# Performance work log

Hardware: AMD Instinct MI355X
Metric: run time of the kernel (lower is better)

Reference implementation:

```python
import jax, jax.numpy as jnp
import numpy as np


def setup_inputs() -> dict:
    key = jax.random.key(0)
    k = jax.random.split(key, 5)
    C, Cb = 128, 64
    x = jax.random.normal(k[0], (8, C, 64, 64), dtype=jnp.float32)
    s_in = 1.0 / np.sqrt(C)
    s_b = 1.0 / np.sqrt(Cb)
    w_theta = jax.random.normal(k[1], (Cb, C), dtype=jnp.float32) * s_in
    w_phi = jax.random.normal(k[2], (Cb, C), dtype=jnp.float32) * s_in
    w_g = jax.random.normal(k[3], (Cb, C), dtype=jnp.float32) * s_in
    w_last = jax.random.normal(k[4], (C, Cb), dtype=jnp.float32) * s_b
    return {"x": x, "w_theta": w_theta, "w_phi": w_phi, "w_g": w_g, "w_last": w_last}


def reference(x, w_theta, w_phi, w_g, w_last):
    B, C, H, W = x.shape
    xf = x.reshape(B, C, H * W)            # [B, C, N]
    theta = jnp.einsum('kc,bcn->bkn', w_theta, xf)   # [B, Cb, N]
    phi = jnp.einsum('kc,bcn->bkn', w_phi, xf)       # [B, Cb, N]
    g = jnp.einsum('kc,bcn->bkn', w_g, xf)           # [B, Cb, N]
    # attention over spatial positions: [B, N, N]
    attn = jax.nn.softmax(jnp.einsum('bkn,bkm->bnm', theta, phi), axis=-1)
    y = jnp.einsum('bnm,bkm->bkn', attn, g)          # [B, Cb, N]
    out = jnp.einsum('ck,bkn->bcn', w_last, y).reshape(B, C, H, W)
    return out + x
```

## Files before the change

### kernel.cpp

```cpp
#include <hip/hip_runtime.h>
#include <stdint.h>

typedef _Float16 h8v __attribute__((ext_vector_type(8)));
typedef _Float16 h4v __attribute__((ext_vector_type(4)));
typedef float f4v __attribute__((ext_vector_type(4)));
typedef _Float16 f16;

#define NB 8
#define CC 128
#define CB 64
#define NN 4096
#define L2E 1.4426950408889634f

#define GLD(gp, lp) __builtin_amdgcn_global_load_lds( \
    (const __attribute__((address_space(1))) void*)(gp), \
    (__attribute__((address_space(3))) void*)(lp), 16, 0, 0)

#define WAITV1() asm volatile("s_waitcnt vmcnt(1)" ::: "memory")
#define WAITV0() asm volatile("s_waitcnt vmcnt(0)" ::: "memory")
#define WAITL0() asm volatile("s_waitcnt lgkmcnt(0)" ::: "memory")

__global__ __launch_bounds__(256) void pack_w(
    const float* __restrict__ wth, const float* __restrict__ wph,
    const float* __restrict__ wg,  const float* __restrict__ wl,
    f16* __restrict__ wthp, f16* __restrict__ wphp,
    f16* __restrict__ wgp,  f16* __restrict__ wlp)
{
    const int t = blockIdx.x * 256 + threadIdx.x;
    for (int i = t; i < 8192; i += 2048){
        const int j = i & 7, lane = (i >> 3) & 63, kc = (i >> 9) & 3, ks = i >> 11;
        const int row = ks * 16 + (lane & 15);
        const int col = kc * 32 + ((lane >> 4) & 3) * 8 + j;
        wthp[i] = (f16)(wth[row * CC + col] * L2E);
        wphp[i] = (f16)(wph[row * CC + col]);
        wgp [i] = (f16)(wg [row * CC + col]);
    }
    for (int i = t; i < 8192; i += 2048){
        const int j = i & 7, lane = (i >> 3) & 63, kc = (i >> 9) & 1, cs = i >> 10;
        const int row = cs * 16 + (lane & 15);
        const int col = kc * 32 + ((lane >> 4) & 3) * 8 + j;
        wlp[i] = (f16)(wl[row * CB + col]);
    }
}

__global__ __launch_bounds__(512) void proj_kernel(
    const float* __restrict__ x, const f16* __restrict__ wthp,
    const f16* __restrict__ wphp, const f16* __restrict__ wgp,
    f16* __restrict__ thetaT, f16* __restrict__ phiT, f16* __restrict__ gbuf)
{
    __shared__ __align__(16) f16 xT[64][136];
    __shared__ __align__(16) f16 rep[8][16 * 72];
    const int b  = blockIdx.x & 7;
    const int n0 = (blockIdx.x >> 3) << 6;
    const int t  = threadIdx.x;

    #pragma unroll
    for (int i = 0; i < 4; i++){
        int v  = t + 512 * i;
        int c  = v >> 4;
        int j0 = (v & 15) << 2;
        const f4v xv = *(const f4v*)&x[((size_t)(b * CC + c)) * NN + n0 + j0];
        #pragma unroll
        for (int jj = 0; jj < 4; jj++) xT[j0 + jj][c] = (f16)xv[jj];
    }
    __syncthreads();

    const int w = t >> 6, lane = t & 63, quad = lane >> 4, l15 = lane & 15;
    const int wq = w & 3, grp = w >> 2;
    const int rrow = lane >> 3, rcol = (lane & 7) * 8;

    h8v bx[4];
    #pragma unroll
    for (int kc = 0; kc < 4; kc++)
        bx[kc] = *(const h8v*)&xT[wq * 16 + l15][kc * 32 + quad * 8];

    {
        const f16* WP = (grp == 0) ? wthp : wphp;
        f16* OUT      = (grp == 0) ? thetaT : phiT;
        for (int ks = 0; ks < 4; ks++){
            f4v acc = {0.f, 0.f, 0.f, 0.f};
            #pragma unroll
            for (int kc = 0; kc < 4; kc++){
                const h8v af = *(const h8v*)&WP[(ks * 4 + kc) * 512 + lane * 8];
                acc = __builtin_amdgcn_mfma_f32_16x16x32_f16(af, bx[kc], acc, 0, 0, 0);
            }
            h4v pv;
            #pragma unroll
            for (int r = 0; r < 4; r++) pv[r] = (f16)acc[r];
            *(h4v*)&rep[w][l15 * 72 + ks * 16 + quad * 4] = pv;
        }
        #pragma unroll
        for (int j = 0; j < 2; j++){
            const h8v vv = *(const h8v*)&rep[w][(rrow + 8 * j) * 72 + rcol];
            *(h8v*)&OUT[((size_t)(b * NN + n0 + wq * 16 + rrow + 8 * j)) * CB + rcol] = vv;
        }
    }
    __syncthreads();

    h8v bw[4];
    #pragma unroll
    for (int kc = 0; kc < 4; kc++)
        bw[kc] = *(const h8v*)&wgp[(wq * 4 + kc) * 512 + lane * 8];
    #pragma unroll
    for (int ns2 = 0; ns2 < 2; ns2++){
        const int ns = grp * 2 + ns2;
        f4v acc = {0.f, 0.f, 0.f, 0.f};
        #pragma unroll
        for (int kc = 0; kc < 4; kc++){
            const h8v af = *(const h8v*)&xT[ns * 16 + l15][kc * 32 + quad * 8];
            acc = __builtin_amdgcn_mfma_f32_16x16x32_f16(af, bw[kc], acc, 0, 0, 0);
        }
        h4v pv;
        #pragma unroll
        for (int r = 0; r < 4; r++) pv[r] = (f16)acc[r];
        *(h4v*)&rep[wq][l15 * 72 + ns * 16 + quad * 4] = pv;
    }
    __syncthreads();
    {
        const int row = rrow + 8 * grp;
        const h8v vv = *(const h8v*)&rep[wq][row * 72 + rcol];
        *(h8v*)&gbuf[((size_t)(b * CB + wq * 16 + row)) * NN + n0 + rcol] = vv;
    }
}

__global__ __launch_bounds__(512, 4) void attn_kernel(
    const f16* __restrict__ thetaT, const f16* __restrict__ phiT,
    const f16* __restrict__ gbuf, const f16* __restrict__ wlp,
    const float* __restrict__ x, float* __restrict__ out)
{
    __shared__ __align__(16) char SM[49152];
    f16*   const PH  = (f16*)SM;
    f16*   const GG  = (f16*)(SM + 24576);
    float* const MG  = (float*)SM;
    float* const ML  = (float*)(SM + 17408);
    float* const FO  = (float*)SM;
    f16*   const YY  = (f16*)(SM + 36864);

    const int b  = blockIdx.x & 7;
    const int q0 = (blockIdx.x >> 3) << 6;
    const int t  = threadIdx.x;
    const int w  = t >> 6;
    const int lane = t & 63, quad = lane >> 4, l15 = lane & 15;
    const int wq = w & 3;
    const int h  = w >> 2;
    const int n0 = q0 + wq * 16;

    const size_t trow = ((size_t)(b * NN + n0 + l15)) * CB;
    const h8v a0 = *(const h8v*)&thetaT[trow + quad * 8];
    const h8v a1 = *(const h8v*)&thetaT[trow + 32 + quad * 8];

    const int srow = t >> 3;
    const int skg  = t & 7;
    const f16* pS = phiT + ((size_t)(b * NN + srow)) * CB + (skg ^ (srow & 7)) * 8;
    const f16* pG = gbuf + ((size_t)(b * CB + srow)) * NN + skg * 8;
    const int sgs = (srow >> 1) & 3;
    const int cA  = (2 * (skg & 3)) & 3;
    const int gdA = (skg >> 2) * 2048 + srow * 32 + ((cA      ^ sgs) * 8) + ((skg >> 1) & 1) * 4;
    const int gdB = (skg >> 2) * 2048 + srow * 32 + (((cA | 1) ^ sgs) * 8) + ((skg >> 1) & 1) * 4;

    const int so0 = (quad ^ (l15 & 7)) * 8;
    const int so1 = so0 ^ 32;
    const int gvs = (quad ^ ((l15 >> 1) & 3)) * 8;

    const f16* const PB0 = PH + h * 2048 + l15 * 64 + so0;
    const f16* const PB1 = PH + h * 2048 + l15 * 64 + so1;
    const f16* const GB  = GG + h * 2048 + l15 * 32 + gvs;
    f16* const WA = GG + gdA;
    f16* const WB = GG + gdB;
    f16* const PD = PH + t * 8;

    h8v gA = *(const h8v*)pG;
    h8v gB = *(const h8v*)(pG + 64);
    GLD(pS,                    PD);
    GLD(pS + (size_t)64 * CB,  PD + 4096);
    pG += 128;
    pS += (size_t)128 * CB;
    {
        h4v lo_, hi_;
        #pragma unroll
        for (int j = 0; j < 4; j++){ lo_[j] = gA[j]; hi_[j] = gA[4 + j]; }
        *(h4v*)&WA[0] = lo_;
        *(h4v*)&WB[0] = hi_;
    }

    float mrun = -1e30f, lrun = 0.f;
    const f4v zf = {0.f, 0.f, 0.f, 0.f};
    f4v o[4];
    #pragma unroll
    for (int tt = 0; tt < 4; tt++) o[tt] = zf;

#define STEPK(RC, V1, DO_W, DO_L, gw, gl) do {                              \
    if (V1) WAITV1(); else WAITV0();                                        \
    WAITL0();                                                               \
    __builtin_amdgcn_s_barrier();                                           \
    asm volatile("" ::: "memory");                                          \
    if (DO_W){                                                              \
        h4v lo_, hi_;                                                       \
        _Pragma("unroll")                                                   \
        for (int j = 0; j < 4; j++){ lo_[j] = gw[j]; hi_[j] = gw[4 + j]; }  \
        *(h4v*)&WA[((RC + 1) % 3) * 4096] = lo_;                            \
        *(h4v*)&WB[((RC + 1) % 3) * 4096] = hi_;                            \
    }                                                                       \
    if (DO_L){                                                              \
        gl = *(const h8v*)pG;  pG += 64;                                    \
        __builtin_amdgcn_sched_barrier(0);                                  \
        GLD(pS, PD + ((RC + 2) % 3) * 4096);                                \
        pS += (size_t)64 * CB;                                              \
    }                                                                       \
    f4v s0_, s1_;                                                           \
    __builtin_amdgcn_s_setprio(1);                                          \
    {                                                                       \
        const h8v pb0 = *(const h8v*)(PB0 + RC * 4096);                     \
        const h8v pb1 = *(const h8v*)(PB1 + RC * 4096);                     \
        f4v sv = zf;                                                        \
        sv = __builtin_amdgcn_mfma_f32_16x16x32_f16(pb0, a0, sv, 0, 0, 0);  \
        sv = __builtin_amdgcn_mfma_f32_16x16x32_f16(pb1, a1, sv, 0, 0, 0);  \
        s0_ = sv;                                                           \
        const h8v pb2 = *(const h8v*)(PB0 + RC * 4096 + 1024);              \
        const h8v pb3 = *(const h8v*)(PB1 + RC * 4096 + 1024);              \
        f4v sw = zf;                                                        \
        sw = __builtin_amdgcn_mfma_f32_16x16x32_f16(pb2, a0, sw, 0, 0, 0);  \
        sw = __builtin_amdgcn_mfma_f32_16x16x32_f16(pb3, a1, sw, 0, 0, 0);  \
        s1_ = sw;                                                           \
    }                                                                       \
    __builtin_amdgcn_s_setprio(0);                                          \
    float smax_ = fmaxf(fmaxf(s0_[0], s0_[1]), fmaxf(s0_[2], s0_[3]));      \
    smax_ = fmaxf(smax_, fmaxf(fmaxf(s1_[0], s1_[1]), fmaxf(s1_[2], s1_[3])));\
    if (__any(smax_ - mrun > 8.f)){                                         \
        smax_ = fmaxf(smax_, __shfl_xor(smax_, 16));                        \
        smax_ = fmaxf(smax_, __shfl_xor(smax_, 32));                        \
        const float mn_ = fmaxf(mrun, smax_);                               \
        const float al_ = __builtin_amdgcn_exp2f(mrun - mn_);               \
        mrun = mn_;                                                         \
        lrun *= al_;                                                        \
        _Pragma("unroll")                                                   \
        for (int tt = 0; tt < 4; tt++)                                      \
            _Pragma("unroll")                                               \
            for (int r = 0; r < 4; r++)                                     \
                o[tt][r] *= al_;                                            \
    }                                                                       \
    float lsum_ = 0.f;                                                      \
    h8v pa_;                                                                \
    _Pragma("unroll")                                                       \
    for (int r = 0; r < 4; r++){                                            \
        float p_ = __builtin_amdgcn_exp2f(s0_[r] - mrun);                   \
        lsum_ += p_;  pa_[r] = (f16)p_;                                     \
        float q_ = __builtin_amdgcn_exp2f(s1_[r] - mrun);                   \
        lsum_ += q_;  pa_[4 + r] = (f16)q_;                                 \
    }                                                                       \
    lrun += lsum_;                                                          \
    __builtin_amdgcn_s_setprio(1);                                          \
    o[0] = __builtin_amdgcn_mfma_f32_16x16x32_f16(                          \
        *(const h8v*)(GB + RC * 4096 +    0), pa_, o[0], 0, 0, 0);          \
    o[1] = __builtin_amdgcn_mfma_f32_16x16x32_f16(                          \
        *(const h8v*)(GB + RC * 4096 +  512), pa_, o[1], 0, 0, 0);          \
    o[2] = __builtin_amdgcn_mfma_f32_16x16x32_f16(                          \
        *(const h8v*)(GB + RC * 4096 + 1024), pa_, o[2], 0, 0, 0);          \
    o[3] = __builtin_amdgcn_mfma_f32_16x16x32_f16(                          \
        *(const h8v*)(GB + RC * 4096 + 1536), pa_, o[3], 0, 0, 0);          \
    __builtin_amdgcn_s_setprio(0);                                          \
} while (0)

    for (int mm = 0; mm < 60; mm += 6){
        STEPK(0, 1, 1, 1, gB, gA);
        STEPK(1, 1, 1, 1, gA, gB);
        STEPK(2, 1, 1, 1, gB, gA);
        STEPK(0, 1, 1, 1, gA, gB);
        STEPK(1, 1, 1, 1, gB, gA);
        STEPK(2, 1, 1, 1, gA, gB);
    }
    STEPK(0, 1, 1, 1, gB, gA);
    STEPK(1, 1, 1, 1, gA, gB);
    STEPK(2, 1, 1, 0, gB, gA);
    STEPK(0, 0, 0, 0, gA, gB);
#undef STEPK

    lrun += __shfl_xor(lrun, 16);
    lrun += __shfl_xor(lrun, 32);

    __syncthreads();

    if (h == 1){
        #pragma unroll
        for (int tt2 = 0; tt2 < 4; tt2++)
            *(f4v*)&MG[wq * 1088 + l15 * 68 + tt2 * 16 + quad * 4] = o[tt2];
        if (lane < 16){
            ML[wq * 32 + lane * 2 + 0] = mrun;
            ML[wq * 32 + lane * 2 + 1] = lrun;
        }
    }
    __syncthreads();

    if (h == 0){
        const float m4 = ML[wq * 32 + l15 * 2 + 0];
        const float l4 = ML[wq * 32 + l15 * 2 + 1];
        const float M  = fmaxf(mrun, m4);
        const float e0 = __builtin_amdgcn_exp2f(mrun - M);
        const float e1 = __builtin_amdgcn_exp2f(m4 - M);
        const float inv = 1.0f / (lrun * e0 + l4 * e1);
        #pragma unroll
        for (int tt2 = 0; tt2 < 4; tt2++){
            const f4v o4 = *(const f4v*)&MG[wq * 1088 + l15 * 68 + tt2 * 16 + quad * 4];
            h4v yv;
            #pragma unroll
            for (int r = 0; r < 4; r++)
                yv[r] = (f16)((o[tt2][r] * e0 + o4[r] * e1) * inv);
            *(h4v*)&YY[(wq * 16 + l15) * 72 + tt2 * 16 + quad * 4] = yv;
        }
    }
    __syncthreads();

    const f4v zf2 = {0.f, 0.f, 0.f, 0.f};
    const h8v yB0 = *(const h8v*)&YY[(wq * 16 + l15) * 72 + quad * 8];
    const h8v yB1 = *(const h8v*)&YY[(wq * 16 + l15) * 72 + 32 + quad * 8];
    #pragma unroll
    for (int ci = 0; ci < 4; ci++){
        const int cs = h * 4 + ci;
        const h8v wa0 = *(const h8v*)&wlp[(cs * 2 + 0) * 512 + lane * 8];
        const h8v wa1 = *(const h8v*)&wlp[(cs * 2 + 1) * 512 + lane * 8];
        f4v acc = zf2;
        acc = __builtin_amdgcn_mfma_f32_16x16x32_f16(wa0, yB0, acc, 0, 0, 0);
        acc = __builtin_amdgcn_mfma_f32_16x16x32_f16(wa1, yB1, acc, 0, 0, 0);
        #pragma unroll
        for (int r = 0; r < 4; r++)
            FO[(cs * 16 + quad * 4 + r) * 68 + wq * 16 + l15] = acc[r];
    }
    __syncthreads();

    #pragma unroll
    for (int i = 0; i < 4; i++){
        const int row = i * 32 + (t >> 4);
        const int nf  = (t & 15) * 4;
        const f4v v = *(const f4v*)&FO[row * 68 + nf];
        const size_t idx = ((size_t)(b * CC + row)) * NN + q0 + nf;
        const f4v xv = *(const f4v*)&x[idx];
        f4v ov;
        #pragma unroll
        for (int r = 0; r < 4; r++) ov[r] = v[r] + xv[r];
        *(f4v*)&out[idx] = ov;
    }
}

extern "C" void kernel_launch(void* const* d_in, const int* in_sizes, int n_in,
                              void* d_out, int out_size, void* d_ws, size_t ws_size,
                              hipStream_t stream)
{
    const float* x   = (const float*)d_in[0];
    const float* wth = (const float*)d_in[1];
    const float* wph = (const float*)d_in[2];
    const float* wg  = (const float*)d_in[3];
    const float* wl  = (const float*)d_in[4];
    float* out = (float*)d_out;

    f16* thetaT = (f16*)d_ws;
    f16* phiT   = thetaT + (size_t)NB * NN * CB;
    f16* gbuf   = phiT   + (size_t)NB * NN * CB;
    f16* wthp   = gbuf   + (size_t)NB * NN * CB;
    f16* wphp   = wthp + 8192;
    f16* wgp    = wphp + 8192;
    f16* wlp    = wgp  + 8192;

    pack_w<<<8, 256, 0, stream>>>(wth, wph, wg, wl, wthp, wphp, wgp, wlp);
    proj_kernel<<<NB * 64, 512, 0, stream>>>(x, wthp, wphp, wgp, thetaT, phiT, gbuf);
    attn_kernel<<<NB * 64, 512, 0, stream>>>(thetaT, phiT, gbuf, wlp, x, out);
}
```

Before: 139.6 us.

## Fuse pack, projection and attention into one cooperative kernel with grid syncs

Merges the three launches (weight packing, projection, attention) into a single cooperative kernel separated by grid-wide barriers, with a fallback to three separate launches if the cooperative launch fails. The aim is to remove kernel launch gaps and tail effects between stages. In exchange it adds two grid syncs, and the projection stage now runs under the attention kernel's launch bounds and shared memory size, which may limit occupancy. The 512 blocks must all be co-resident for the cooperative launch to succeed.

```diff
diff --git a/kernel.cpp b/kernel.cpp
--- a/kernel.cpp
+++ b/kernel.cpp
@@ -1,5 +1,8 @@
 #include <hip/hip_runtime.h>
+#include <hip/hip_cooperative_groups.h>
 #include <stdint.h>
+
+namespace cg = cooperative_groups;
 
 typedef _Float16 h8v __attribute__((ext_vector_type(8)));
 typedef _Float16 h4v __attribute__((ext_vector_type(4)));
@@ -20,39 +23,40 @@
 #define WAITV0() asm volatile("s_waitcnt vmcnt(0)" ::: "memory")
 #define WAITL0() asm volatile("s_waitcnt lgkmcnt(0)" ::: "memory")
 
-__global__ __launch_bounds__(256) void pack_w(
+__device__ __forceinline__ void pack_body(int tg,
     const float* __restrict__ wth, const float* __restrict__ wph,
     const float* __restrict__ wg,  const float* __restrict__ wl,
     f16* __restrict__ wthp, f16* __restrict__ wphp,
     f16* __restrict__ wgp,  f16* __restrict__ wlp)
 {
-    const int t = blockIdx.x * 256 + threadIdx.x;
-    for (int i = t; i < 8192; i += 2048){
-        const int j = i & 7, lane = (i >> 3) & 63, kc = (i >> 9) & 3, ks = i >> 11;
-        const int row = ks * 16 + (lane & 15);
-        const int col = kc * 32 + ((lane >> 4) & 3) * 8 + j;
-        wthp[i] = (f16)(wth[row * CC + col] * L2E);
-        wphp[i] = (f16)(wph[row * CC + col]);
-        wgp [i] = (f16)(wg [row * CC + col]);
-    }
-    for (int i = t; i < 8192; i += 2048){
-        const int j = i & 7, lane = (i >> 3) & 63, kc = (i >> 9) & 1, cs = i >> 10;
-        const int row = cs * 16 + (lane & 15);
-        const int col = kc * 32 + ((lane >> 4) & 3) * 8 + j;
-        wlp[i] = (f16)(wl[row * CB + col]);
-    }
-}
-
-__global__ __launch_bounds__(512) void proj_kernel(
+    if (tg < 8192){
+        const int i = tg;
+        {
+            const int j = i & 7, lane = (i >> 3) & 63, kc = (i >> 9) & 3, ks = i >> 11;
+            const int row = ks * 16 + (lane & 15);
+            const int col = kc * 32 + ((lane >> 4) & 3) * 8 + j;
+            wthp[i] = (f16)(wth[row * CC + col] * L2E);
+            wphp[i] = (f16)(wph[row * CC + col]);
+            wgp [i] = (f16)(wg [row * CC + col]);
+        }
+        {
+            const int j = i & 7, lane = (i >> 3) & 63, kc = (i >> 9) & 1, cs = i >> 10;
+            const int row = cs * 16 + (lane & 15);
+            const int col = kc * 32 + ((lane >> 4) & 3) * 8 + j;
+            wlp[i] = (f16)(wl[row * CB + col]);
+        }
+    }
+}
+
+__device__ __forceinline__ void proj_body(char* SM, int bid, int t,
     const float* __restrict__ x, const f16* __restrict__ wthp,
     const f16* __restrict__ wphp, const f16* __restrict__ wgp,
     f16* __restrict__ thetaT, f16* __restrict__ phiT, f16* __restrict__ gbuf)
 {
-    __shared__ __align__(16) f16 xT[64][136];
-    __shared__ __align__(16) f16 rep[8][16 * 72];
-    const int b  = blockIdx.x & 7;
-    const int n0 = (blockIdx.x >> 3) << 6;
-    const int t  = threadIdx.x;
+    f16 (*xT)[136] = (f16(*)[136])SM;
+    f16* rep = (f16*)(SM + 17408);
+    const int b  = bid & 7;
+    const int n0 = (bid >> 3) << 6;
 
     #pragma unroll
     for (int i = 0; i < 4; i++){
@@ -87,11 +91,11 @@
             h4v pv;
             #pragma unroll
             for (int r = 0; r < 4; r++) pv[r] = (f16)acc[r];
-            *(h4v*)&rep[w][l15 * 72 + ks * 16 + quad * 4] = pv;
+            *(h4v*)&rep[w * 1152 + l15 * 72 + ks * 16 + quad * 4] = pv;
         }
         #pragma unroll
         for (int j = 0; j < 2; j++){
-            const h8v vv = *(const h8v*)&rep[w][(rrow + 8 * j) * 72 + rcol];
+            const h8v vv = *(const h8v*)&rep[w * 1152 + (rrow + 8 * j) * 72 + rcol];
             *(h8v*)&OUT[((size_t)(b * NN + n0 + wq * 16 + rrow + 8 * j)) * CB + rcol] = vv;
         }
     }
@@ -113,22 +117,21 @@
         h4v pv;
         #pragma unroll
         for (int r = 0; r < 4; r++) pv[r] = (f16)acc[r];
-        *(h4v*)&rep[wq][l15 * 72 + ns * 16 + quad * 4] = pv;
+        *(h4v*)&rep[wq * 1152 + l15 * 72 + ns * 16 + quad * 4] = pv;
     }
     __syncthreads();
     {
         const int row = rrow + 8 * grp;
-        const h8v vv = *(const h8v*)&rep[wq][row * 72 + rcol];
+        const h8v vv = *(const h8v*)&rep[wq * 1152 + row * 72 + rcol];
         *(h8v*)&gbuf[((size_t)(b * CB + wq * 16 + row)) * NN + n0 + rcol] = vv;
     }
 }
 
-__global__ __launch_bounds__(512, 4) void attn_kernel(
+__device__ __forceinline__ void attn_body(char* SM, int bid, int t,
     const f16* __restrict__ thetaT, const f16* __restrict__ phiT,
     const f16* __restrict__ gbuf, const f16* __restrict__ wlp,
     const float* __restrict__ x, float* __restrict__ out)
 {
-    __shared__ __align__(16) char SM[49152];
     f16*   const PH  = (f16*)SM;
     f16*   const GG  = (f16*)(SM + 24576);
     float* const MG  = (float*)SM;
@@ -136,9 +139,8 @@
     float* const FO  = (float*)SM;
     f16*   const YY  = (f16*)(SM + 36864);
 
-    const int b  = blockIdx.x & 7;
-    const int q0 = (blockIdx.x >> 3) << 6;
-    const int t  = threadIdx.x;
+    const int b  = bid & 7;
+    const int q0 = (bid >> 3) << 6;
     const int w  = t >> 6;
     const int lane = t & 63, quad = lane >> 4, l15 = lane & 15;
     const int wq = w & 3;
@@ -341,6 +343,56 @@
     }
 }
 
+__global__ __launch_bounds__(512, 4) void fused_kernel(
+    const float* __restrict__ x,
+    const float* __restrict__ wth, const float* __restrict__ wph,
+    const float* __restrict__ wg,  const float* __restrict__ wl,
+    float* __restrict__ out,
+    f16* __restrict__ thetaT, f16* __restrict__ phiT, f16* __restrict__ gbuf,
+    f16* __restrict__ wthp, f16* __restrict__ wphp,
+    f16* __restrict__ wgp,  f16* __restrict__ wlp)
+{
+    __shared__ __align__(16) char SM[49152];
+    const int bid = blockIdx.x, t = threadIdx.x;
+
+    pack_body(bid * 512 + t, wth, wph, wg, wl, wthp, wphp, wgp, wlp);
+    __threadfence();
+    cg::this_grid().sync();
+
+    proj_body(SM, bid, t, x, wthp, wphp, wgp, thetaT, phiT, gbuf);
+    __threadfence();
+    cg::this_grid().sync();
+
+    attn_body(SM, bid, t, thetaT, phiT, gbuf, wlp, x, out);
+}
+
+__global__ __launch_bounds__(512) void pack_k(
+    const float* __restrict__ wth, const float* __restrict__ wph,
+    const float* __restrict__ wg,  const float* __restrict__ wl,
+    f16* __restrict__ wthp, f16* __restrict__ wphp,
+    f16* __restrict__ wgp,  f16* __restrict__ wlp)
+{
+    pack_body(blockIdx.x * 512 + threadIdx.x, wth, wph, wg, wl, wthp, wphp, wgp, wlp);
+}
+
+__global__ __launch_bounds__(512) void proj_k(
+    const float* __restrict__ x, const f16* __restrict__ wthp,
+    const f16* __restrict__ wphp, const f16* __restrict__ wgp,
+    f16* __restrict__ thetaT, f16* __restrict__ phiT, f16* __restrict__ gbuf)
+{
+    __shared__ __align__(16) char SM[36864];
+    proj_body(SM, blockIdx.x, threadIdx.x, x, wthp, wphp, wgp, thetaT, phiT, gbuf);
+}
+
+__global__ __launch_bounds__(512, 4) void attn_k(
+    const f16* __restrict__ thetaT, const f16* __restrict__ phiT,
+    const f16* __restrict__ gbuf, const f16* __restrict__ wlp,
+    const float* __restrict__ x, float* __restrict__ out)
+{
+    __shared__ __align__(16) char SM[49152];
+    attn_body(SM, blockIdx.x, threadIdx.x, thetaT, phiT, gbuf, wlp, x, out);
+}
+
 extern "C" void kernel_launch(void* const* d_in, const int* in_sizes, int n_in,
                               void* d_out, int out_size, void* d_ws, size_t ws_size,
                               hipStream_t stream)
@@ -360,7 +412,17 @@
     f16* wgp    = wphp + 8192;
     f16* wlp    = wgp  + 8192;
 
-    pack_w<<<8, 256, 0, stream>>>(wth, wph, wg, wl, wthp, wphp, wgp, wlp);
-    proj_kernel<<<NB * 64, 512, 0, stream>>>(x, wthp, wphp, wgp, thetaT, phiT, gbuf);
-    attn_kernel<<<NB * 64, 512, 0, stream>>>(thetaT, phiT, gbuf, wlp, x, out);
-}
+    void* args[] = {
+        (void*)&x, (void*)&wth, (void*)&wph, (void*)&wg, (void*)&wl,
+        (void*)&out, (void*)&thetaT, (void*)&phiT, (void*)&gbuf,
+        (void*)&wthp, (void*)&wphp, (void*)&wgp, (void*)&wlp
+    };
+    hipError_t e = hipLaunchCooperativeKernel((const void*)fused_kernel,
+                                              dim3(NB * 64), dim3(512),
+                                              args, 0, stream);
+    if (e != hipSuccess){
+        pack_k<<<16, 512, 0, stream>>>(wth, wph, wg, wl, wthp, wphp, wgp, wlp);
+        proj_k<<<NB * 64, 512, 0, stream>>>(x, wthp, wphp, wgp, thetaT, phiT, gbuf);
+        attn_k<<<NB * 64, 512, 0, stream>>>(thetaT, phiT, gbuf, wlp, x, out);
+    }
+}
```

Result: slower. 371.6 us (+166.3%).

## Process 128-key tiles per attention step and fold weight packing into consumers

Applied to the files above, without the earlier changes.

Each attention pipeline step now handles 128 keys instead of 64, with the phi and g LDS buffers enlarged (LDS grows to 80KB) and slot indices rotated to match. This halves the number of barriers and waitcnt points per key sweep and gives more MFMA work per sync. Separately, the pack_w kernel launch is removed, and the proj and attn kernels load fp32 weights directly and convert them to fp16 in registers. The larger LDS footprint may cut the number of resident blocks per CU, and the weight conversion becomes redundant per-block work.

```diff
diff --git a/kernel.cpp b/kernel.cpp
--- a/kernel.cpp
+++ b/kernel.cpp
@@ -16,36 +16,13 @@
     (const __attribute__((address_space(1))) void*)(gp), \
     (__attribute__((address_space(3))) void*)(lp), 16, 0, 0)
 
-#define WAITV1() asm volatile("s_waitcnt vmcnt(1)" ::: "memory")
+#define WAITV2() asm volatile("s_waitcnt vmcnt(2)" ::: "memory")
 #define WAITV0() asm volatile("s_waitcnt vmcnt(0)" ::: "memory")
 #define WAITL0() asm volatile("s_waitcnt lgkmcnt(0)" ::: "memory")
 
-__global__ __launch_bounds__(256) void pack_w(
-    const float* __restrict__ wth, const float* __restrict__ wph,
-    const float* __restrict__ wg,  const float* __restrict__ wl,
-    f16* __restrict__ wthp, f16* __restrict__ wphp,
-    f16* __restrict__ wgp,  f16* __restrict__ wlp)
-{
-    const int t = blockIdx.x * 256 + threadIdx.x;
-    for (int i = t; i < 8192; i += 2048){
-        const int j = i & 7, lane = (i >> 3) & 63, kc = (i >> 9) & 3, ks = i >> 11;
-        const int row = ks * 16 + (lane & 15);
-        const int col = kc * 32 + ((lane >> 4) & 3) * 8 + j;
-        wthp[i] = (f16)(wth[row * CC + col] * L2E);
-        wphp[i] = (f16)(wph[row * CC + col]);
-        wgp [i] = (f16)(wg [row * CC + col]);
-    }
-    for (int i = t; i < 8192; i += 2048){
-        const int j = i & 7, lane = (i >> 3) & 63, kc = (i >> 9) & 1, cs = i >> 10;
-        const int row = cs * 16 + (lane & 15);
-        const int col = kc * 32 + ((lane >> 4) & 3) * 8 + j;
-        wlp[i] = (f16)(wl[row * CB + col]);
-    }
-}
-
 __global__ __launch_bounds__(512) void proj_kernel(
-    const float* __restrict__ x, const f16* __restrict__ wthp,
-    const f16* __restrict__ wphp, const f16* __restrict__ wgp,
+    const float* __restrict__ x, const float* __restrict__ wth,
+    const float* __restrict__ wph, const float* __restrict__ wg,
     f16* __restrict__ thetaT, f16* __restrict__ phiT, f16* __restrict__ gbuf)
 {
     __shared__ __align__(16) f16 xT[64][136];
@@ -75,13 +52,22 @@
         bx[kc] = *(const h8v*)&xT[wq * 16 + l15][kc * 32 + quad * 8];
 
     {
-        const f16* WP = (grp == 0) ? wthp : wphp;
-        f16* OUT      = (grp == 0) ? thetaT : phiT;
+        const float* WF = (grp == 0) ? wth : wph;
+        const float sc = (grp == 0) ? L2E : 1.0f;
+        f16* OUT       = (grp == 0) ? thetaT : phiT;
         for (int ks = 0; ks < 4; ks++){
             f4v acc = {0.f, 0.f, 0.f, 0.f};
             #pragma unroll
             for (int kc = 0; kc < 4; kc++){
-                const h8v af = *(const h8v*)&WP[(ks * 4 + kc) * 512 + lane * 8];
+                const float* wr = WF + (ks * 16 + l15) * CC + kc * 32 + quad * 8;
+                const f4v wa = *(const f4v*)wr;
+                const f4v wb = *(const f4v*)(wr + 4);
+                h8v af;
+                #pragma unroll
+                for (int j = 0; j < 4; j++){
+                    af[j]     = (f16)(wa[j] * sc);
+                    af[4 + j] = (f16)(wb[j] * sc);
+                }
                 acc = __builtin_amdgcn_mfma_f32_16x16x32_f16(af, bx[kc], acc, 0, 0, 0);
             }
             h4v pv;
@@ -99,8 +85,16 @@
 
     h8v bw[4];
     #pragma unroll
-    for (int kc = 0; kc < 4; kc++)
-        bw[kc] = *(const h8v*)&wgp[(wq * 4 + kc) * 512 + lane * 8];
+    for (int kc = 0; kc < 4; kc++){
+        const float* wr = wg + (wq * 16 + l15) * CC + kc * 32 + quad * 8;
+        const f4v wa = *(const f4v*)wr;
+        const f4v wb = *(const f4v*)(wr + 4);
+        #pragma unroll
+        for (int j = 0; j < 4; j++){
+            bw[kc][j]     = (f16)wa[j];
+            bw[kc][4 + j] = (f16)wb[j];
+        }
+    }
     #pragma unroll
     for (int ns2 = 0; ns2 < 2; ns2++){
         const int ns = grp * 2 + ns2;
@@ -125,12 +119,12 @@
 
 __global__ __launch_bounds__(512, 4) void attn_kernel(
     const f16* __restrict__ thetaT, const f16* __restrict__ phiT,
-    const f16* __restrict__ gbuf, const f16* __restrict__ wlp,
+    const f16* __restrict__ gbuf, const float* __restrict__ wl,
     const float* __restrict__ x, float* __restrict__ out)
 {
-    __shared__ __align__(16) char SM[49152];
+    __shared__ __align__(16) char SM[81920];
     f16*   const PH  = (f16*)SM;
-    f16*   const GG  = (f16*)(SM + 24576);
+    f16*   const GG  = (f16*)(SM + 49152);
     float* const MG  = (float*)SM;
     float* const ML  = (float*)(SM + 17408);
     float* const FO  = (float*)SM;
@@ -169,18 +163,25 @@
     f16* const WB = GG + gdB;
     f16* const PD = PH + t * 8;
 
-    h8v gA = *(const h8v*)pG;
-    h8v gB = *(const h8v*)(pG + 64);
-    GLD(pS,                    PD);
-    GLD(pS + (size_t)64 * CB,  PD + 4096);
-    pG += 128;
-    pS += (size_t)128 * CB;
+    h8v gA0 = *(const h8v*)pG;
+    h8v gA1 = *(const h8v*)(pG + 64);
+    h8v gB0 = *(const h8v*)(pG + 128);
+    h8v gB1 = *(const h8v*)(pG + 192);
+    pG += 256;
+    GLD(pS,                     PD);
+    GLD(pS + (size_t) 64 * CB,  PD + 4096);
+    GLD(pS + (size_t)128 * CB,  PD + 8192);
+    GLD(pS + (size_t)192 * CB,  PD + 12288);
+    pS += (size_t)256 * CB;
     {
-        h4v lo_, hi_;
-        #pragma unroll
-        for (int j = 0; j < 4; j++){ lo_[j] = gA[j]; hi_[j] = gA[4 + j]; }
-        *(h4v*)&WA[0] = lo_;
-        *(h4v*)&WB[0] = hi_;
+        h4v l0_, h0_, l1_, h1_;
+        #pragma unroll
+        for (int j = 0; j < 4; j++){
+            l0_[j] = gA0[j]; h0_[j] = gA0[4 + j];
+            l1_[j] = gA1[j]; h1_[j] = gA1[4 + j];
+        }
+        *(h4v*)&WA[0]    = l0_;  *(h4v*)&WB[0]    = h0_;
+        *(h4v*)&WA[4096] = l1_;  *(h4v*)&WB[4096] = h1_;
     }
 
     float mrun = -1e30f, lrun = 0.f;
@@ -189,43 +190,65 @@
     #pragma unroll
     for (int tt = 0; tt < 4; tt++) o[tt] = zf;
 
-#define STEPK(RC, V1, DO_W, DO_L, gw, gl) do {                              \
-    if (V1) WAITV1(); else WAITV0();                                        \
+#define STEPK128(SL3, SL2R, SL2W, SLD, V2, DO_W, DO_L, gw0, gw1, gl0, gl1) do { \
+    if (V2) WAITV2(); else WAITV0();                                        \
     WAITL0();                                                               \
     __builtin_amdgcn_s_barrier();                                           \
     asm volatile("" ::: "memory");                                          \
     if (DO_W){                                                              \
-        h4v lo_, hi_;                                                       \
+        h4v l0_, h0_, l1_, h1_;                                             \
         _Pragma("unroll")                                                   \
-        for (int j = 0; j < 4; j++){ lo_[j] = gw[j]; hi_[j] = gw[4 + j]; }  \
-        *(h4v*)&WA[((RC + 1) % 3) * 4096] = lo_;                            \
-        *(h4v*)&WB[((RC + 1) % 3) * 4096] = hi_;                            \
+        for (int j = 0; j < 4; j++){                                        \
+            l0_[j] = gw0[j]; h0_[j] = gw0[4 + j];                           \
+            l1_[j] = gw1[j]; h1_[j] = gw1[4 + j];                           \
+        }                                                                   \
+        *(h4v*)&WA[SL2W * 8192]        = l0_;                               \
+        *(h4v*)&WB[SL2W * 8192]        = h0_;                               \
+        *(h4v*)&WA[SL2W * 8192 + 4096] = l1_;                               \
+        *(h4v*)&WB[SL2W * 8192 + 4096] = h1_;                               \
     }                                                                       \
     if (DO_L){                                                              \
-        gl = *(const h8v*)pG;  pG += 64;                                    \
+        gl0 = *(const h8v*)pG;                                              \
+        gl1 = *(const h8v*)(pG + 64);                                       \
+        pG += 128;                                                          \
         __builtin_amdgcn_sched_barrier(0);                                  \
-        GLD(pS, PD + ((RC + 2) % 3) * 4096);                                \
-        pS += (size_t)64 * CB;                                              \
+        GLD(pS,                   PD + SLD * 8192);                         \
+        GLD(pS + (size_t)64 * CB, PD + SLD * 8192 + 4096);                  \
+        pS += (size_t)128 * CB;                                             \
     }                                                                       \
-    f4v s0_, s1_;                                                           \
+    f4v s0_, s1_, s2_, s3_;                                                 \
     __builtin_amdgcn_s_setprio(1);                                          \
     {                                                                       \
-        const h8v pb0 = *(const h8v*)(PB0 + RC * 4096);                     \
-        const h8v pb1 = *(const h8v*)(PB1 + RC * 4096);                     \
         f4v sv = zf;                                                        \
-        sv = __builtin_amdgcn_mfma_f32_16x16x32_f16(pb0, a0, sv, 0, 0, 0);  \
-        sv = __builtin_amdgcn_mfma_f32_16x16x32_f16(pb1, a1, sv, 0, 0, 0);  \
+        sv = __builtin_amdgcn_mfma_f32_16x16x32_f16(                        \
+            *(const h8v*)(PB0 + SL3 * 8192), a0, sv, 0, 0, 0);              \
+        sv = __builtin_amdgcn_mfma_f32_16x16x32_f16(                        \
+            *(const h8v*)(PB1 + SL3 * 8192), a1, sv, 0, 0, 0);              \
         s0_ = sv;                                                           \
-        const h8v pb2 = *(const h8v*)(PB0 + RC * 4096 + 1024);              \
-        const h8v pb3 = *(const h8v*)(PB1 + RC * 4096 + 1024);              \
         f4v sw = zf;                                                        \
-        sw = __builtin_amdgcn_mfma_f32_16x16x32_f16(pb2, a0, sw, 0, 0, 0);  \
-        sw = __builtin_amdgcn_mfma_f32_16x16x32_f16(pb3, a1, sw, 0, 0, 0);  \
+        sw = __builtin_amdgcn_mfma_f32_16x16x32_f16(                        \
+            *(const h8v*)(PB0 + SL3 * 8192 + 1024), a0, sw, 0, 0, 0);       \
+        sw = __builtin_amdgcn_mfma_f32_16x16x32_f16(                        \
+            *(const h8v*)(PB1 + SL3 * 8192 + 1024), a1, sw, 0, 0, 0);       \
         s1_ = sw;                                                           \
+        f4v sx = zf;                                                        \
+        sx = __builtin_amdgcn_mfma_f32_16x16x32_f16(                        \
+            *(const h8v*)(PB0 + SL3 * 8192 + 4096), a0, sx, 0, 0, 0);       \
+        sx = __builtin_amdgcn_mfma_f32_16x16x32_f16(                        \
+            *(const h8v*)(PB1 + SL3 * 8192 + 4096), a1, sx, 0, 0, 0);       \
+        s2_ = sx;                                                           \
+        f4v sy = zf;                                                        \
+        sy = __builtin_amdgcn_mfma_f32_16x16x32_f16(                        \
+            *(const h8v*)(PB0 + SL3 * 8192 + 5120), a0, sy, 0, 0, 0);       \
+        sy = __builtin_amdgcn_mfma_f32_16x16x32_f16(                        \
+            *(const h8v*)(PB1 + SL3 * 8192 + 5120), a1, sy, 0, 0, 0);       \
+        s3_ = sy;                                                           \
     }                                                                       \
     __builtin_amdgcn_s_setprio(0);                                          \
     float smax_ = fmaxf(fmaxf(s0_[0], s0_[1]), fmaxf(s0_[2], s0_[3]));      \
     smax_ = fmaxf(smax_, fmaxf(fmaxf(s1_[0], s1_[1]), fmaxf(s1_[2], s1_[3])));\
+    smax_ = fmaxf(smax_, fmaxf(fmaxf(s2_[0], s2_[1]), fmaxf(s2_[2], s2_[3])));\
+    smax_ = fmaxf(smax_, fmaxf(fmaxf(s3_[0], s3_[1]), fmaxf(s3_[2], s3_[3])));\
     if (__any(smax_ - mrun > 8.f)){                                         \
         smax_ = fmaxf(smax_, __shfl_xor(smax_, 16));                        \
         smax_ = fmaxf(smax_, __shfl_xor(smax_, 32));                        \
@@ -240,40 +263,50 @@
                 o[tt][r] *= al_;                                            \
     }                                                                       \
     float lsum_ = 0.f;                                                      \
-    h8v pa_;                                                                \
+    h8v pa0_, pa1_;                                                         \
     _Pragma("unroll")                                                       \
     for (int r = 0; r < 4; r++){                                            \
         float p_ = __builtin_amdgcn_exp2f(s0_[r] - mrun);                   \
-        lsum_ += p_;  pa_[r] = (f16)p_;                                     \
+        lsum_ += p_;  pa0_[r] = (f16)p_;                                    \
         float q_ = __builtin_amdgcn_exp2f(s1_[r] - mrun);                   \
-        lsum_ += q_;  pa_[4 + r] = (f16)q_;                                 \
+        lsum_ += q_;  pa0_[4 + r] = (f16)q_;                                \
+        float u_ = __builtin_amdgcn_exp2f(s2_[r] - mrun);                   \
+        lsum_ += u_;  pa1_[r] = (f16)u_;                                    \
+        float v_ = __builtin_amdgcn_exp2f(s3_[r] - mrun);                   \
+        lsum_ += v_;  pa1_[4 + r] = (f16)v_;                                \
     }                                                                       \
     lrun += lsum_;                                                          \
     __builtin_amdgcn_s_setprio(1);                                          \
     o[0] = __builtin_amdgcn_mfma_f32_16x16x32_f16(                          \
-        *(const h8v*)(GB + RC * 4096 +    0), pa_, o[0], 0, 0, 0);          \
+        *(const h8v*)(GB + SL2R * 8192 +    0), pa0_, o[0], 0, 0, 0);       \
     o[1] = __builtin_amdgcn_mfma_f32_16x16x32_f16(                          \
-        *(const h8v*)(GB + RC * 4096 +  512), pa_, o[1], 0, 0, 0);          \
+        *(const h8v*)(GB + SL2R * 8192 +  512), pa0_, o[1], 0, 0, 0);       \
     o[2] = __builtin_amdgcn_mfma_f32_16x16x32_f16(                          \
-        *(const h8v*)(GB + RC * 4096 + 1024), pa_, o[2], 0, 0, 0);          \
+        *(const h8v*)(GB + SL2R * 8192 + 1024), pa0_, o[2], 0, 0, 0);       \
     o[3] = __builtin_amdgcn_mfma_f32_16x16x32_f16(                          \
-        *(const h8v*)(GB + RC * 4096 + 1536), pa_, o[3], 0, 0, 0);          \
+        *(const h8v*)(GB + SL2R * 8192 + 1536), pa0_, o[3], 0, 0, 0);       \
+    o[0] = __builtin_amdgcn_mfma_f32_16x16x32_f16(                          \
+        *(const h8v*)(GB + SL2R * 8192 + 4096), pa1_, o[0], 0, 0, 0);       \
+    o[1] = __builtin_amdgcn_mfma_f32_16x16x32_f16(                          \
+        *(const h8v*)(GB + SL2R * 8192 + 4608), pa1_, o[1], 0, 0, 0);       \
+    o[2] = __builtin_amdgcn_mfma_f32_16x16x32_f16(                          \
+        *(const h8v*)(GB + SL2R * 8192 + 5120), pa1_, o[2], 0, 0, 0);       \
+    o[3] = __builtin_amdgcn_mfma_f32_16x16x32_f16(                          \
+        *(const h8v*)(GB + SL2R * 8192 + 5632), pa1_, o[3], 0, 0, 0);       \
     __builtin_amdgcn_s_setprio(0);                                          \
 } while (0)
 
-    for (int mm = 0; mm < 60; mm += 6){
-        STEPK(0, 1, 1, 1, gB, gA);
-        STEPK(1, 1, 1, 1, gA, gB);
-        STEPK(2, 1, 1, 1, gB, gA);
-        STEPK(0, 1, 1, 1, gA, gB);
-        STEPK(1, 1, 1, 1, gB, gA);
-        STEPK(2, 1, 1, 1, gA, gB);
-    }
-    STEPK(0, 1, 1, 1, gB, gA);
-    STEPK(1, 1, 1, 1, gA, gB);
-    STEPK(2, 1, 1, 0, gB, gA);
-    STEPK(0, 0, 0, 0, gA, gB);
-#undef STEPK
+    for (int mm = 0; mm < 30; mm += 6){
+        STEPK128(0, 0, 1, 2, 1, 1, 1, gB0, gB1, gA0, gA1);
+        STEPK128(1, 1, 0, 0, 1, 1, 1, gA0, gA1, gB0, gB1);
+        STEPK128(2, 0, 1, 1, 1, 1, 1, gB0, gB1, gA0, gA1);
+        STEPK128(0, 1, 0, 2, 1, 1, 1, gA0, gA1, gB0, gB1);
+        STEPK128(1, 0, 1, 0, 1, 1, 1, gB0, gB1, gA0, gA1);
+        STEPK128(2, 1, 0, 1, 1, 1, 1, gA0, gA1, gB0, gB1);
+    }
+    STEPK128(0, 0, 1, 2, 1, 1, 0, gB0, gB1, gA0, gA1);
+    STEPK128(1, 1, 0, 0, 0, 0, 0, gA0, gA1, gB0, gB1);
+#undef STEPK128
 
     lrun += __shfl_xor(lrun, 16);
     lrun += __shfl_xor(lrun, 32);
@@ -316,8 +349,19 @@
     #pragma unroll
     for (int ci = 0; ci < 4; ci++){
         const int cs = h * 4 + ci;
-        const h8v wa0 = *(const h8v*)&wlp[(cs * 2 + 0) * 512 + lane * 8];
-        const h8v wa1 = *(const h8v*)&wlp[(cs * 2 + 1) * 512 + lane * 8];
+        const float* wrow = wl + (cs * 16 + l15) * CB + quad * 8;
+        const f4v wA0 = *(const f4v*)(wrow);
+        const f4v wA1 = *(const f4v*)(wrow + 4);
+        const f4v wB0 = *(const f4v*)(wrow + 32);
+        const f4v wB1 = *(const f4v*)(wrow + 36);
+        h8v wa0, wa1;
+        #pragma unroll
+        for (int j = 0; j < 4; j++){
+            wa0[j]     = (f16)wA0[j];
+            wa0[4 + j] = (f16)wA1[j];
+            wa1[j]     = (f16)wB0[j];
+            wa1[4 + j] = (f16)wB1[j];
+        }
         f4v acc = zf2;
         acc = __builtin_amdgcn_mfma_f32_16x16x32_f16(wa0, yB0, acc, 0, 0, 0);
         acc = __builtin_amdgcn_mfma_f32_16x16x32_f16(wa1, yB1, acc, 0, 0, 0);
@@ -355,12 +399,7 @@
     f16* thetaT = (f16*)d_ws;
     f16* phiT   = thetaT + (size_t)NB * NN * CB;
     f16* gbuf   = phiT   + (size_t)NB * NN * CB;
-    f16* wthp   = gbuf   + (size_t)NB * NN * CB;
-    f16* wphp   = wthp + 8192;
-    f16* wgp    = wphp + 8192;
-    f16* wlp    = wgp  + 8192;
-
-    pack_w<<<8, 256, 0, stream>>>(wth, wph, wg, wl, wthp, wphp, wgp, wlp);
-    proj_kernel<<<NB * 64, 512, 0, stream>>>(x, wthp, wphp, wgp, thetaT, phiT, gbuf);
-    attn_kernel<<<NB * 64, 512, 0, stream>>>(thetaT, phiT, gbuf, wlp, x, out);
+
+    proj_kernel<<<NB * 64, 512, 0, stream>>>(x, wth, wph, wg, thetaT, phiT, gbuf);
+    attn_kernel<<<NB * 64, 512, 0, stream>>>(thetaT, phiT, gbuf, wl, x, out);
 }
```

New measurement: 155.4 us. 11.4% more time.
